# Kernel tuning notes

Hardware: AMD Instinct MI355X
Metric: run time of the kernel (lower is better)

Reference implementation:

```python
import jax, jax.numpy as jnp
import numpy as np
from jax import lax

B, C, H, W = 2, 192, 256, 256
HEADS = 4
EPS = 1e-12  # F.normalize clamp_min eps


def conv1x1(w, x):
    # w: [O, I, 1, 1], x: [B, I, H, W] -> [B, O, H, W]
    return jnp.einsum('oi,bihw->bohw', w[:, :, 0, 0], x)


def setup_inputs() -> dict:
    key = jax.random.key(0)
    ks = jax.random.split(key, 8)
    s = 0.05
    return {
        'x': jax.random.normal(ks[0], (B, C, H, W), dtype=jnp.float32),
        'noise_map': jax.random.uniform(ks[1], (B, 1, 1, 1), dtype=jnp.float32),
        'base_temp': jnp.ones((HEADS, 1, 1), dtype=jnp.float32),
        'w_nm1': jax.random.normal(ks[2], (C // 4, 1, 1, 1), dtype=jnp.float32) * s,
        'w_nm2': jax.random.normal(ks[3], (HEADS, C // 4, 1, 1), dtype=jnp.float32) * s,
        'w_qkv': jax.random.normal(ks[4], (3 * C, C, 1, 1), dtype=jnp.float32) * s,
        'w_dw': jax.random.normal(ks[5], (3 * C, 1, 3, 3), dtype=jnp.float32) * s,
        'w_out': jax.random.normal(ks[6], (C, C, 1, 1), dtype=jnp.float32) * s,
    }


def reference(x, noise_map, base_temp, w_nm1, w_nm2, w_qkv, w_dw, w_out):
    b, c, h, w = x.shape
    ch = c // HEADS  # channels per head

    # qkv 1x1 conv followed by depthwise 3x3 conv
    qkv = conv1x1(w_qkv, x)
    qkv = lax.conv_general_dilated(
        qkv, w_dw, window_strides=(1, 1), padding='SAME',
        feature_group_count=3 * c,
        dimension_numbers=('NCHW', 'OIHW', 'NCHW'))
    q, k, v = jnp.split(qkv, 3, axis=1)

    def heads(t):  # [b, c, h, w] -> [b, head, ch, h*w]
        return t.reshape(b, HEADS, ch, h * w)

    q, k, v = heads(q), heads(k), heads(v)

    # L2 normalize over spatial dim (matches F.normalize eps clamp)
    q = q / jnp.maximum(jnp.linalg.norm(q, axis=-1, keepdims=True), EPS)
    k = k / jnp.maximum(jnp.linalg.norm(k, axis=-1, keepdims=True), EPS)

    # noise modulation MLP (1x1 convs on [b,1,1,1] noise map)
    nm = conv1x1(w_nm1, noise_map)
    nm = jnp.where(nm >= 0, nm, 0.2 * nm)  # LeakyReLU(0.2)
    nm = jax.nn.sigmoid(conv1x1(w_nm2, nm))  # [b, heads, 1, 1]
    noise_weight = nm.reshape(b, HEADS, 1, 1)
    temp = base_temp[None] * (2.0 - noise_weight)  # [b, heads, 1, 1]

    # channel (transposed) attention: [b, head, ch, ch]
    attn = jnp.einsum('bhcn,bhdn->bhcd', q, k) * temp
    attn = jax.nn.softmax(attn, axis=-1)
    out = jnp.einsum('bhcd,bhdn->bhcn', attn, v)

    out = out.reshape(b, c, h, w)
    return conv1x1(w_out, out)
```

## Files before the change

### kernel.cpp

```cpp
#include <hip/hip_runtime.h>
#include <hip/hip_bf16.h>

#define NPIX 65536
#define IW 256

typedef unsigned short ushort_t;
typedef __attribute__((ext_vector_type(8))) short bf16x8;
typedef __attribute__((ext_vector_type(4))) float f32x4;

__device__ __forceinline__ float b2f(ushort_t u) {
    union { unsigned int i; float f; } v;
    v.i = ((unsigned int)u) << 16;
    return v.f;
}
__device__ __forceinline__ ushort_t f2b(float f) {
    __hip_bfloat16 h = __float2bfloat16(f);
    return *reinterpret_cast<ushort_t*>(&h);
}

template<int B_F32, int A_BF16, int OUT_BF16>
__global__ __launch_bounds__(256) void kgemm_fused(const void* __restrict__ Aptr,
                                                   const void* __restrict__ Bsrc,
                                                   void* __restrict__ Cout,
                                                   int mtiles) {
    __shared__ ushort_t Bs[128 * 200];
    __shared__ ushort_t AsLu[64 * 200];
    const int tid = threadIdx.x;
    const int lane = tid & 63;
    const int wave = tid >> 6;
    const long n_base = (long)blockIdx.x * 128;

    ushort_t (*Lu)[66] = reinterpret_cast<ushort_t (*)[66]>(AsLu);
    #pragma unroll
    for (int half = 0; half < 2; half++) {
        const long n0 = n_base + half * 64;
        __syncthreads();
        #pragma unroll
        for (int i = 0; i < 24; i++) {
            int e = tid + i * 256;
            int k = e >> 5, n2 = e & 31;
            ushort2 o;
            if (B_F32) {
                float2 v = *reinterpret_cast<const float2*>(
                    (const float*)Bsrc + (long)k * NPIX + n0 + n2 * 2);
                o = make_ushort2(f2b(v.x), f2b(v.y));
            } else {
                o = *reinterpret_cast<const ushort2*>(
                    (const ushort_t*)Bsrc + (long)k * NPIX + n0 + n2 * 2);
            }
            *reinterpret_cast<ushort2*>(&Lu[k][n2 * 2]) = o;
        }
        __syncthreads();
        const int n = tid >> 2, seg = tid & 3;
        const int kb = seg * 48;
        ushort_t* dst = &Bs[(half * 64 + n) * 200 + kb];
        #pragma unroll
        for (int w = 0; w < 6; w++) {
            unsigned int p0 = (unsigned int)Lu[kb + w * 8 + 0][n] | ((unsigned int)Lu[kb + w * 8 + 1][n] << 16);
            unsigned int p1 = (unsigned int)Lu[kb + w * 8 + 2][n] | ((unsigned int)Lu[kb + w * 8 + 3][n] << 16);
            unsigned int p2 = (unsigned int)Lu[kb + w * 8 + 4][n] | ((unsigned int)Lu[kb + w * 8 + 5][n] << 16);
            unsigned int p3 = (unsigned int)Lu[kb + w * 8 + 6][n] | ((unsigned int)Lu[kb + w * 8 + 7][n] << 16);
            *reinterpret_cast<int4*>(dst + w * 8) = make_int4(p0, p1, p2, p3);
        }
    }

    const int r15 = lane & 15;
    const int g8 = (lane >> 4) * 8;
    const int gq = (lane >> 4) * 4;
    const int nw = wave * 32;

    for (int mt = 0; mt < mtiles; mt++) {
        const int m_base = mt * 64;
        __syncthreads();
        #pragma unroll
        for (int i = 0; i < 12; i++) {
            int c = tid + i * 256;
            int m = c / 48, k4 = c % 48;
            if (A_BF16) {
                const ushort_t* A = (const ushort_t*)Aptr;
                ushort4 v = *reinterpret_cast<const ushort4*>(A + (long)(m_base + m) * 192 + k4 * 4);
                *reinterpret_cast<ushort4*>(&AsLu[m * 200 + k4 * 4]) = v;
            } else {
                const float* A = (const float*)Aptr;
                float4 v = *reinterpret_cast<const float4*>(A + (long)(m_base + m) * 192 + k4 * 4);
                ushort4 o = make_ushort4(f2b(v.x), f2b(v.y), f2b(v.z), f2b(v.w));
                *reinterpret_cast<ushort4*>(&AsLu[m * 200 + k4 * 4]) = o;
            }
        }
        __syncthreads();

        f32x4 acc[4][2];
        #pragma unroll
        for (int mi = 0; mi < 4; mi++)
            #pragma unroll
            for (int ni = 0; ni < 2; ni++)
                acc[mi][ni] = (f32x4){0.f, 0.f, 0.f, 0.f};

        #pragma unroll
        for (int kk = 0; kk < 192; kk += 32) {
            bf16x8 a[4], b[2];
            #pragma unroll
            for (int mi = 0; mi < 4; mi++)
                a[mi] = *reinterpret_cast<const bf16x8*>(&AsLu[(mi * 16 + r15) * 200 + kk + g8]);
            #pragma unroll
            for (int ni = 0; ni < 2; ni++)
                b[ni] = *reinterpret_cast<const bf16x8*>(&Bs[(nw + ni * 16 + r15) * 200 + kk + g8]);
            #pragma unroll
            for (int mi = 0; mi < 4; mi++)
                #pragma unroll
                for (int ni = 0; ni < 2; ni++)
                    acc[mi][ni] = __builtin_amdgcn_mfma_f32_16x16x32_bf16(a[mi], b[ni], acc[mi][ni], 0, 0, 0);
        }

        #pragma unroll
        for (int mi = 0; mi < 4; mi++)
            #pragma unroll
            for (int ni = 0; ni < 2; ni++)
                #pragma unroll
                for (int r = 0; r < 4; r++) {
                    long m = m_base + mi * 16 + gq + r;
                    long n = n_base + nw + ni * 16 + r15;
                    if (OUT_BF16) ((ushort_t*)Cout)[m * NPIX + n] = f2b(acc[mi][ni][r]);
                    else          ((float*)Cout)[m * NPIX + n] = acc[mi][ni][r];
                }
    }
}

__global__ __launch_bounds__(256) void kdw_conv(const ushort_t* __restrict__ qkvb,
                                                const float* __restrict__ wdw,
                                                ushort_t* __restrict__ dwb,
                                                ushort_t* __restrict__ dwv) {
    __shared__ ushort_t rows[18][IW];
    const int tid = threadIdx.x;
    const int j = blockIdx.y;
    const int y0 = blockIdx.x * 16;
    const ushort_t* src = qkvb + (long)j * NPIX;
    ushort_t* dst = (j < 384) ? (dwb + (long)j * NPIX) : (dwv + (long)(j - 384) * NPIX);
    float wv[9];
    #pragma unroll
    for (int t = 0; t < 9; t++) wv[t] = wdw[j * 9 + t];

    for (int e = tid; e < 18 * 64; e += 256) {
        int r = e >> 6, x4 = e & 63;
        int yy = y0 - 1 + r;
        ushort4 val = (yy >= 0 && yy <= 255)
            ? *reinterpret_cast<const ushort4*>(src + yy * IW + x4 * 4)
            : make_ushort4(0, 0, 0, 0);
        *reinterpret_cast<ushort4*>(&rows[r][x4 * 4]) = val;
    }
    __syncthreads();

    const int ty = tid >> 4;
    const int tx = (tid & 15) * 16;
    float win[3][18];
    #pragma unroll
    for (int dy = 0; dy < 3; dy++) {
        const ushort_t* rw = rows[ty + dy];
        win[dy][0] = (tx > 0) ? b2f(rw[tx - 1]) : 0.f;
        #pragma unroll
        for (int i = 0; i < 16; i++) win[dy][i + 1] = b2f(rw[tx + i]);
        win[dy][17] = (tx < 240) ? b2f(rw[tx + 16]) : 0.f;
    }

    unsigned int packed[8];
    #pragma unroll
    for (int p2 = 0; p2 < 8; p2++) {
        unsigned int pk = 0;
        #pragma unroll
        for (int half = 0; half < 2; half++) {
            const int p = p2 * 2 + half;
            float a = 0.f;
            #pragma unroll
            for (int dy = 0; dy < 3; dy++)
                #pragma unroll
                for (int dx = 0; dx < 3; dx++)
                    a += wv[dy * 3 + dx] * win[dy][p + dx];
            pk |= ((unsigned int)f2b(a)) << (16 * half);
        }
        packed[p2] = pk;
    }
    int4* dp = reinterpret_cast<int4*>(dst + (y0 + ty) * IW + tx);
    dp[0] = make_int4(packed[0], packed[1], packed[2], packed[3]);
    dp[1] = make_int4(packed[4], packed[5], packed[6], packed[7]);
}

__global__ __launch_bounds__(256) void k2_gram_mfma(const ushort_t* __restrict__ dwb,
                                                    float* __restrict__ Spt,
                                                    float* __restrict__ sqp) {
    const int tid = threadIdx.x;
    const int lane = tid & 63;
    const int wave = tid >> 6;
    const int chunk = blockIdx.x;
    const int h = blockIdx.y;
    const int r15 = lane & 15;
    const int g = lane >> 4;
    const long n0 = (long)chunk * 1024 + wave * 256;
    const ushort_t* qb = dwb + (long)(h * 48) * NPIX + n0;
    const ushort_t* kb = dwb + (long)(192 + h * 48) * NPIX + n0;

    f32x4 acc[3][3];
    #pragma unroll
    for (int mi = 0; mi < 3; mi++)
        #pragma unroll
        for (int nj = 0; nj < 3; nj++)
            acc[mi][nj] = (f32x4){0.f, 0.f, 0.f, 0.f};
    float ssq[3] = {0.f, 0.f, 0.f}, ssk[3] = {0.f, 0.f, 0.f};

    for (int ks = 0; ks < 8; ks++) {
        const int off = ks * 32 + g * 8;
        bf16x8 a[3], bfr[3];
        #pragma unroll
        for (int mi = 0; mi < 3; mi++)
            a[mi] = *reinterpret_cast<const bf16x8*>(qb + (long)(mi * 16 + r15) * NPIX + off);
        #pragma unroll
        for (int nj = 0; nj < 3; nj++)
            bfr[nj] = *reinterpret_cast<const bf16x8*>(kb + (long)(nj * 16 + r15) * NPIX + off);
        #pragma unroll
        for (int mi = 0; mi < 3; mi++)
            #pragma unroll
            for (int j = 0; j < 8; j++) {
                float f = b2f((ushort_t)a[mi][j]);
                ssq[mi] += f * f;
            }
        #pragma unroll
        for (int nj = 0; nj < 3; nj++)
            #pragma unroll
            for (int j = 0; j < 8; j++) {
                float f = b2f((ushort_t)bfr[nj][j]);
                ssk[nj] += f * f;
            }
        #pragma unroll
        for (int mi = 0; mi < 3; mi++)
            #pragma unroll
            for (int nj = 0; nj < 3; nj++)
                acc[mi][nj] = __builtin_amdgcn_mfma_f32_16x16x32_bf16(a[mi], bfr[nj], acc[mi][nj], 0, 0, 0);
    }

    const int cw = chunk * 4 + wave;
    float* outb = Spt + (long)cw * 9216 + h * 2304;
    const int gq = g * 4;
    #pragma unroll
    for (int mi = 0; mi < 3; mi++)
        #pragma unroll
        for (int nj = 0; nj < 3; nj++)
            #pragma unroll
            for (int r = 0; r < 4; r++)
                outb[(mi * 16 + gq + r) * 48 + nj * 16 + r15] = acc[mi][nj][r];

    #pragma unroll
    for (int mi = 0; mi < 3; mi++) {
        ssq[mi] += __shfl_xor(ssq[mi], 16, 64);
        ssq[mi] += __shfl_xor(ssq[mi], 32, 64);
        ssk[mi] += __shfl_xor(ssk[mi], 16, 64);
        ssk[mi] += __shfl_xor(ssk[mi], 32, 64);
    }
    if (lane < 16) {
        float* sqb = sqp + (long)cw * 384;
        #pragma unroll
        for (int mi = 0; mi < 3; mi++) {
            sqb[h * 48 + mi * 16 + lane] = ssq[mi];
            sqb[192 + h * 48 + mi * 16 + lane] = ssk[mi];
        }
    }
}

__global__ __launch_bounds__(256) void k3a_reduce2(const float* __restrict__ Spt,
                                                   const float* __restrict__ sqp,
                                                   float* __restrict__ S1,
                                                   float* __restrict__ sq1) {
    const int seg = blockIdx.y;
    const int w = blockIdx.x * 256 + threadIdx.x;
    if (w < 9216) {
        const float* p = Spt + (long)seg * 32 * 9216 + w;
        float s = 0.f;
        for (int i = 0; i < 32; i++) s += p[(long)i * 9216];
        S1[seg * 9216 + w] = s;
    } else if (w < 9600) {
        const int c = w - 9216;
        const float* p = sqp + (long)seg * 32 * 384 + c;
        float s = 0.f;
        for (int i = 0; i < 32; i++) s += p[i * 384];
        sq1[seg * 384 + c] = s;
    }
}

__global__ __launch_bounds__(256) void k3b_attn(const float* __restrict__ S1,
                                                const float* __restrict__ sq1,
                                                const float* __restrict__ noise,
                                                const float* __restrict__ btemp,
                                                const float* __restrict__ w_nm1,
                                                const float* __restrict__ w_nm2,
                                                float* __restrict__ attn, int b) {
    __shared__ float sA[48][49];
    __shared__ float invq[48], invk[48];
    __shared__ float stemp;
    const int h = blockIdx.x, tid = threadIdx.x;
    for (int e = tid; e < 2304; e += 256) {
        float s = 0.f;
        #pragma unroll
        for (int seg = 0; seg < 8; seg++) s += S1[seg * 9216 + h * 2304 + e];
        sA[e / 48][e % 48] = s;
    }
    if (tid < 96) {
        int c = (tid < 48) ? (h * 48 + tid) : (192 + h * 48 + (tid - 48));
        float s = 0.f;
        #pragma unroll
        for (int seg = 0; seg < 8; seg++) s += sq1[seg * 384 + c];
        float inv = 1.f / fmaxf(sqrtf(s), 1e-12f);
        if (tid < 48) invq[tid] = inv; else invk[tid - 48] = inv;
    }
    if (tid == 0) {
        float nz = noise[b];
        float a = 0.f;
        for (int i = 0; i < 48; i++) {
            float t = w_nm1[i] * nz;
            t = (t >= 0.f) ? t : 0.2f * t;
            a += w_nm2[h * 48 + i] * t;
        }
        float sig = 1.f / (1.f + expf(-a));
        stemp = btemp[h] * (2.f - sig);
    }
    __syncthreads();
    for (int e = tid; e < 2304; e += 256) {
        int c = e / 48, d = e % 48;
        sA[c][d] *= invq[c] * invk[d] * stemp;
    }
    __syncthreads();
    if (tid < 48) {
        float m = -1e30f;
        for (int d = 0; d < 48; d++) m = fmaxf(m, sA[tid][d]);
        float sum = 0.f;
        for (int d = 0; d < 48; d++) {
            float e_ = expf(sA[tid][d] - m);
            sA[tid][d] = e_;
            sum += e_;
        }
        float r = 1.f / sum;
        for (int d = 0; d < 48; d++)
            attn[h * 2304 + tid * 48 + d] = sA[tid][d] * r;
    }
}

__global__ __launch_bounds__(256) void k4_weff(const float* __restrict__ w_out,
                                               const float* __restrict__ attn,
                                               ushort_t* __restrict__ weffb) {
    int e = blockIdx.x * 256 + threadIdx.x;
    int o = e / 192, j = e % 192;
    int h = j / 48, d = j % 48;
    const float* wr = w_out + o * 192 + h * 48;
    const float* ar = attn + h * 2304 + d;
    float s = 0.f;
    #pragma unroll
    for (int c = 0; c < 48; c++) s += wr[c] * ar[c * 48];
    weffb[e] = f2b(s);
}

extern "C" void kernel_launch(void* const* d_in, const int* in_sizes, int n_in,
                              void* d_out, int out_size, void* d_ws, size_t ws_size,
                              hipStream_t stream) {
    const float* x      = (const float*)d_in[0];
    const float* noise  = (const float*)d_in[1];
    const float* btemp  = (const float*)d_in[2];
    const float* w_nm1  = (const float*)d_in[3];
    const float* w_nm2  = (const float*)d_in[4];
    const float* w_qkv  = (const float*)d_in[5];
    const float* w_dw   = (const float*)d_in[6];
    const float* w_out  = (const float*)d_in[7];
    float* out = (float*)d_out;
    float* ws = (float*)d_ws;

    ushort_t* qkvb = (ushort_t*)ws;
    float* Spt  = ws;
    float* sqp  = ws + 9437184;
    float* S1   = ws + 9830400;
    float* sq1  = ws + 9904128;
    float* attn = ws + 9907200;
    ushort_t* weffb = (ushort_t*)(ws + 9916416);
    ushort_t* dwv = (ushort_t*)(ws + 18874368);
    ushort_t* dwb = (ushort_t*)(ws + 25427968);

    for (int b = 0; b < 2; b++) {
        const float* xb = x + (long)b * 192 * NPIX;
        float* outb = out + (long)b * 192 * NPIX;
        kgemm_fused<1, 0, 1><<<512, 256, 0, stream>>>(w_qkv, xb, qkvb, 9);
        kdw_conv<<<dim3(16, 576), 256, 0, stream>>>(qkvb, w_dw, dwb, dwv);
        k2_gram_mfma<<<dim3(64, 4), 256, 0, stream>>>(dwb, Spt, sqp);
        k3a_reduce2<<<dim3(38, 8), 256, 0, stream>>>(Spt, sqp, S1, sq1);
        k3b_attn<<<4, 256, 0, stream>>>(S1, sq1, noise, btemp, w_nm1, w_nm2, attn, b);
        k4_weff<<<144, 256, 0, stream>>>(w_out, attn, weffb);
        kgemm_fused<0, 1, 0><<<512, 256, 0, stream>>>(weffb, dwv, outb, 3);
    }
}
```

Before: 239.5 us.

## Batch both images into single kernel launches and fuse attention with weff

Adds a batch grid dimension with per-tensor strides to every kernel so both batch items run in one launch each, when the workspace is large enough to hold both images' intermediates. It also folds the effective-weight computation (w_out times attention) into the attention softmax kernel, which removes one launch and the global round-trip of the attn matrix. This cuts launch count from 14 to 6, doubles the grid per launch to improve occupancy of small kernels, and drops the serialization between batches. The cost is a larger workspace, and the code falls back to the old per-batch loop if the workspace is too small.

```diff
diff --git a/kernel.cpp b/kernel.cpp
--- a/kernel.cpp
+++ b/kernel.cpp
@@ -22,12 +22,13 @@
 __global__ __launch_bounds__(256) void kgemm_fused(const void* __restrict__ Aptr,
                                                    const void* __restrict__ Bsrc,
                                                    void* __restrict__ Cout,
-                                                   int mtiles) {
+                                                   int mtiles, long Astr, long Bstr, long Cstr) {
     __shared__ ushort_t Bs[128 * 200];
     __shared__ ushort_t AsLu[64 * 200];
     const int tid = threadIdx.x;
     const int lane = tid & 63;
     const int wave = tid >> 6;
+    const int batch = blockIdx.y;
     const long n_base = (long)blockIdx.x * 128;
 
     ushort_t (*Lu)[66] = reinterpret_cast<ushort_t (*)[66]>(AsLu);
@@ -42,11 +43,11 @@
             ushort2 o;
             if (B_F32) {
                 float2 v = *reinterpret_cast<const float2*>(
-                    (const float*)Bsrc + (long)k * NPIX + n0 + n2 * 2);
+                    (const float*)Bsrc + batch * Bstr + (long)k * NPIX + n0 + n2 * 2);
                 o = make_ushort2(f2b(v.x), f2b(v.y));
             } else {
                 o = *reinterpret_cast<const ushort2*>(
-                    (const ushort_t*)Bsrc + (long)k * NPIX + n0 + n2 * 2);
+                    (const ushort_t*)Bsrc + batch * Bstr + (long)k * NPIX + n0 + n2 * 2);
             }
             *reinterpret_cast<ushort2*>(&Lu[k][n2 * 2]) = o;
         }
@@ -77,11 +78,11 @@
             int c = tid + i * 256;
             int m = c / 48, k4 = c % 48;
             if (A_BF16) {
-                const ushort_t* A = (const ushort_t*)Aptr;
+                const ushort_t* A = (const ushort_t*)Aptr + batch * Astr;
                 ushort4 v = *reinterpret_cast<const ushort4*>(A + (long)(m_base + m) * 192 + k4 * 4);
                 *reinterpret_cast<ushort4*>(&AsLu[m * 200 + k4 * 4]) = v;
             } else {
-                const float* A = (const float*)Aptr;
+                const float* A = (const float*)Aptr + batch * Astr;
                 float4 v = *reinterpret_cast<const float4*>(A + (long)(m_base + m) * 192 + k4 * 4);
                 ushort4 o = make_ushort4(f2b(v.x), f2b(v.y), f2b(v.z), f2b(v.w));
                 *reinterpret_cast<ushort4*>(&AsLu[m * 200 + k4 * 4]) = o;
@@ -120,8 +121,8 @@
                 for (int r = 0; r < 4; r++) {
                     long m = m_base + mi * 16 + gq + r;
                     long n = n_base + nw + ni * 16 + r15;
-                    if (OUT_BF16) ((ushort_t*)Cout)[m * NPIX + n] = f2b(acc[mi][ni][r]);
-                    else          ((float*)Cout)[m * NPIX + n] = acc[mi][ni][r];
+                    if (OUT_BF16) ((ushort_t*)Cout)[batch * Cstr + m * NPIX + n] = f2b(acc[mi][ni][r]);
+                    else          ((float*)Cout)[batch * Cstr + m * NPIX + n] = acc[mi][ni][r];
                 }
     }
 }
@@ -129,13 +130,16 @@
 __global__ __launch_bounds__(256) void kdw_conv(const ushort_t* __restrict__ qkvb,
                                                 const float* __restrict__ wdw,
                                                 ushort_t* __restrict__ dwb,
-                                                ushort_t* __restrict__ dwv) {
+                                                ushort_t* __restrict__ dwv,
+                                                long qstr, long dbstr, long dvstr) {
     __shared__ ushort_t rows[18][IW];
     const int tid = threadIdx.x;
     const int j = blockIdx.y;
+    const int batch = blockIdx.z;
     const int y0 = blockIdx.x * 16;
-    const ushort_t* src = qkvb + (long)j * NPIX;
-    ushort_t* dst = (j < 384) ? (dwb + (long)j * NPIX) : (dwv + (long)(j - 384) * NPIX);
+    const ushort_t* src = qkvb + batch * qstr + (long)j * NPIX;
+    ushort_t* dst = (j < 384) ? (dwb + batch * dbstr + (long)j * NPIX)
+                              : (dwv + batch * dvstr + (long)(j - 384) * NPIX);
     float wv[9];
     #pragma unroll
     for (int t = 0; t < 9; t++) wv[t] = wdw[j * 9 + t];
@@ -186,17 +190,19 @@
 
 __global__ __launch_bounds__(256) void k2_gram_mfma(const ushort_t* __restrict__ dwb,
                                                     float* __restrict__ Spt,
-                                                    float* __restrict__ sqp) {
+                                                    float* __restrict__ sqp,
+                                                    long dbstr, long Sptstr, long sqpstr) {
     const int tid = threadIdx.x;
     const int lane = tid & 63;
     const int wave = tid >> 6;
     const int chunk = blockIdx.x;
     const int h = blockIdx.y;
+    const int batch = blockIdx.z;
     const int r15 = lane & 15;
     const int g = lane >> 4;
     const long n0 = (long)chunk * 1024 + wave * 256;
-    const ushort_t* qb = dwb + (long)(h * 48) * NPIX + n0;
-    const ushort_t* kb = dwb + (long)(192 + h * 48) * NPIX + n0;
+    const ushort_t* qb = dwb + batch * dbstr + (long)(h * 48) * NPIX + n0;
+    const ushort_t* kb = dwb + batch * dbstr + (long)(192 + h * 48) * NPIX + n0;
 
     f32x4 acc[3][3];
     #pragma unroll
@@ -237,7 +243,7 @@
     }
 
     const int cw = chunk * 4 + wave;
-    float* outb = Spt + (long)cw * 9216 + h * 2304;
+    float* outb = Spt + batch * Sptstr + (long)cw * 9216 + h * 2304;
     const int gq = g * 4;
     #pragma unroll
     for (int mi = 0; mi < 3; mi++)
@@ -255,7 +261,7 @@
         ssk[mi] += __shfl_xor(ssk[mi], 32, 64);
     }
     if (lane < 16) {
-        float* sqb = sqp + (long)cw * 384;
+        float* sqb = sqp + batch * sqpstr + (long)cw * 384;
         #pragma unroll
         for (int mi = 0; mi < 3; mi++) {
             sqb[h * 48 + mi * 16 + lane] = ssq[mi];
@@ -267,50 +273,56 @@
 __global__ __launch_bounds__(256) void k3a_reduce2(const float* __restrict__ Spt,
                                                    const float* __restrict__ sqp,
                                                    float* __restrict__ S1,
-                                                   float* __restrict__ sq1) {
+                                                   float* __restrict__ sq1,
+                                                   long Sptstr, long sqpstr, long S1str, long sq1str) {
     const int seg = blockIdx.y;
+    const int batch = blockIdx.z;
     const int w = blockIdx.x * 256 + threadIdx.x;
     if (w < 9216) {
-        const float* p = Spt + (long)seg * 32 * 9216 + w;
+        const float* p = Spt + batch * Sptstr + (long)seg * 32 * 9216 + w;
         float s = 0.f;
         for (int i = 0; i < 32; i++) s += p[(long)i * 9216];
-        S1[seg * 9216 + w] = s;
+        S1[batch * S1str + seg * 9216 + w] = s;
     } else if (w < 9600) {
         const int c = w - 9216;
-        const float* p = sqp + (long)seg * 32 * 384 + c;
+        const float* p = sqp + batch * sqpstr + (long)seg * 32 * 384 + c;
         float s = 0.f;
         for (int i = 0; i < 32; i++) s += p[i * 384];
-        sq1[seg * 384 + c] = s;
-    }
-}
-
-__global__ __launch_bounds__(256) void k3b_attn(const float* __restrict__ S1,
-                                                const float* __restrict__ sq1,
-                                                const float* __restrict__ noise,
-                                                const float* __restrict__ btemp,
-                                                const float* __restrict__ w_nm1,
-                                                const float* __restrict__ w_nm2,
-                                                float* __restrict__ attn, int b) {
+        sq1[batch * sq1str + seg * 384 + c] = s;
+    }
+}
+
+__global__ __launch_bounds__(256) void k3b_attn_weff(const float* __restrict__ S1,
+                                                     const float* __restrict__ sq1,
+                                                     const float* __restrict__ noise,
+                                                     const float* __restrict__ btemp,
+                                                     const float* __restrict__ w_nm1,
+                                                     const float* __restrict__ w_nm2,
+                                                     const float* __restrict__ w_out,
+                                                     ushort_t* __restrict__ weffb,
+                                                     int b0, long S1str, long sq1str, long wstr) {
     __shared__ float sA[48][49];
     __shared__ float invq[48], invk[48];
     __shared__ float stemp;
-    const int h = blockIdx.x, tid = threadIdx.x;
+    const int h = blockIdx.x, batch = blockIdx.y, tid = threadIdx.x;
+    const float* S1b = S1 + batch * S1str;
+    const float* sq1b = sq1 + batch * sq1str;
     for (int e = tid; e < 2304; e += 256) {
         float s = 0.f;
         #pragma unroll
-        for (int seg = 0; seg < 8; seg++) s += S1[seg * 9216 + h * 2304 + e];
+        for (int seg = 0; seg < 8; seg++) s += S1b[seg * 9216 + h * 2304 + e];
         sA[e / 48][e % 48] = s;
     }
     if (tid < 96) {
         int c = (tid < 48) ? (h * 48 + tid) : (192 + h * 48 + (tid - 48));
         float s = 0.f;
         #pragma unroll
-        for (int seg = 0; seg < 8; seg++) s += sq1[seg * 384 + c];
+        for (int seg = 0; seg < 8; seg++) s += sq1b[seg * 384 + c];
         float inv = 1.f / fmaxf(sqrtf(s), 1e-12f);
         if (tid < 48) invq[tid] = inv; else invk[tid - 48] = inv;
     }
     if (tid == 0) {
-        float nz = noise[b];
+        float nz = noise[b0 + batch];
         float a = 0.f;
         for (int i = 0; i < 48; i++) {
             float t = w_nm1[i] * nz;
@@ -336,23 +348,18 @@
             sum += e_;
         }
         float r = 1.f / sum;
-        for (int d = 0; d < 48; d++)
-            attn[h * 2304 + tid * 48 + d] = sA[tid][d] * r;
-    }
-}
-
-__global__ __launch_bounds__(256) void k4_weff(const float* __restrict__ w_out,
-                                               const float* __restrict__ attn,
-                                               ushort_t* __restrict__ weffb) {
-    int e = blockIdx.x * 256 + threadIdx.x;
-    int o = e / 192, j = e % 192;
-    int h = j / 48, d = j % 48;
-    const float* wr = w_out + o * 192 + h * 48;
-    const float* ar = attn + h * 2304 + d;
-    float s = 0.f;
-    #pragma unroll
-    for (int c = 0; c < 48; c++) s += wr[c] * ar[c * 48];
-    weffb[e] = f2b(s);
+        for (int d = 0; d < 48; d++) sA[tid][d] *= r;
+    }
+    __syncthreads();
+    ushort_t* wb = weffb + batch * wstr;
+    for (int e = tid; e < 9216; e += 256) {
+        int o = e / 48, d = e % 48;
+        const float* wr = w_out + o * 192 + h * 48;
+        float s = 0.f;
+        #pragma unroll
+        for (int c = 0; c < 48; c++) s += wr[c] * sA[c][d];
+        wb[o * 192 + h * 48 + d] = f2b(s);
+    }
 }
 
 extern "C" void kernel_launch(void* const* d_in, const int* in_sizes, int n_in,
@@ -369,25 +376,54 @@
     float* out = (float*)d_out;
     float* ws = (float*)d_ws;
 
-    ushort_t* qkvb = (ushort_t*)ws;
-    float* Spt  = ws;
-    float* sqp  = ws + 9437184;
-    float* S1   = ws + 9830400;
-    float* sq1  = ws + 9904128;
-    float* attn = ws + 9907200;
-    ushort_t* weffb = (ushort_t*)(ws + 9916416);
-    ushort_t* dwv = (ushort_t*)(ws + 18874368);
-    ushort_t* dwb = (ushort_t*)(ws + 25427968);
-
-    for (int b = 0; b < 2; b++) {
-        const float* xb = x + (long)b * 192 * NPIX;
-        float* outb = out + (long)b * 192 * NPIX;
-        kgemm_fused<1, 0, 1><<<512, 256, 0, stream>>>(w_qkv, xb, qkvb, 9);
-        kdw_conv<<<dim3(16, 576), 256, 0, stream>>>(qkvb, w_dw, dwb, dwv);
-        k2_gram_mfma<<<dim3(64, 4), 256, 0, stream>>>(dwb, Spt, sqp);
-        k3a_reduce2<<<dim3(38, 8), 256, 0, stream>>>(Spt, sqp, S1, sq1);
-        k3b_attn<<<4, 256, 0, stream>>>(S1, sq1, noise, btemp, w_nm1, w_nm2, attn, b);
-        k4_weff<<<144, 256, 0, stream>>>(w_out, attn, weffb);
-        kgemm_fused<0, 1, 0><<<512, 256, 0, stream>>>(weffb, dwv, outb, 3);
-    }
-}
+    const long need2 = 80603136L;
+    if ((long)(ws_size / 4) >= need2) {
+        ushort_t* qkvb = (ushort_t*)ws;
+        ushort_t* dwv  = (ushort_t*)(ws + 37748736);
+        ushort_t* dwb  = (ushort_t*)(ws + 50331648);
+        float* Spt  = ws + 75497472;
+        float* sqp  = ws + 80216064;
+        float* S1   = ws + 80412672;
+        float* sq1  = ws + 80560128;
+        ushort_t* weffb = (ushort_t*)(ws + 80566272);
+
+        kgemm_fused<1, 0, 1><<<dim3(512, 2), 256, 0, stream>>>(
+            w_qkv, x, qkvb, 9, 0L, 192L * NPIX, 576L * NPIX);
+        kdw_conv<<<dim3(16, 576, 2), 256, 0, stream>>>(
+            qkvb, w_dw, dwb, dwv, 576L * NPIX, 384L * NPIX, 192L * NPIX);
+        k2_gram_mfma<<<dim3(64, 4, 2), 256, 0, stream>>>(
+            dwb, Spt, sqp, 384L * NPIX, 2359296L, 98304L);
+        k3a_reduce2<<<dim3(38, 8, 2), 256, 0, stream>>>(
+            Spt, sqp, S1, sq1, 2359296L, 98304L, 73728L, 3072L);
+        k3b_attn_weff<<<dim3(4, 2), 256, 0, stream>>>(
+            S1, sq1, noise, btemp, w_nm1, w_nm2, w_out, weffb, 0, 73728L, 3072L, 36864L);
+        kgemm_fused<0, 1, 0><<<dim3(512, 2), 256, 0, stream>>>(
+            weffb, dwv, out, 3, 36864L, 192L * NPIX, 192L * NPIX);
+    } else {
+        ushort_t* qkvb = (ushort_t*)ws;
+        float* Spt  = ws;
+        float* sqp  = ws + 9437184;
+        float* S1   = ws + 9830400;
+        float* sq1  = ws + 9904128;
+        ushort_t* weffb = (ushort_t*)(ws + 9907200);
+        ushort_t* dwv = (ushort_t*)(ws + 18874368);
+        ushort_t* dwb = (ushort_t*)(ws + 25427968);
+
+        for (int b = 0; b < 2; b++) {
+            const float* xb = x + (long)b * 192 * NPIX;
+            float* outb = out + (long)b * 192 * NPIX;
+            kgemm_fused<1, 0, 1><<<dim3(512, 1), 256, 0, stream>>>(
+                w_qkv, xb, qkvb, 9, 0L, 0L, 0L);
+            kdw_conv<<<dim3(16, 576, 1), 256, 0, stream>>>(
+                qkvb, w_dw, dwb, dwv, 0L, 0L, 0L);
+            k2_gram_mfma<<<dim3(64, 4, 1), 256, 0, stream>>>(
+                dwb, Spt, sqp, 0L, 0L, 0L);
+            k3a_reduce2<<<dim3(38, 8, 1), 256, 0, stream>>>(
+                Spt, sqp, S1, sq1, 0L, 0L, 0L, 0L);
+            k3b_attn_weff<<<dim3(4, 1), 256, 0, stream>>>(
+                S1, sq1, noise, btemp, w_nm1, w_nm2, w_out, weffb, b, 0L, 0L, 0L);
+            kgemm_fused<0, 1, 0><<<dim3(512, 1), 256, 0, stream>>>(
+                weffb, dwv, outb, 3, 0L, 0L, 0L);
+        }
+    }
+}
```

Measured after the change: 250.1 us. 1.04x slower.
